# Kernel tuning notes

Hardware: AMD Instinct MI355X
Metric: run time of the kernel (lower is better)

The kernel has to match this reference:

```python
import jax, jax.numpy as jnp
import numpy as np

N, E, F_IN, F_E, EMB, G = 25000, 100000, 32, 8, 32, 512


def _nnconv(x, src, dst, ea, w1, b1, w2, b2, root, bias):
    # edge MLP: [E,F_E] -> [E,16] -> [E, in*EMB] -> per-edge weight matrix [E,in,EMB]
    h = jax.nn.relu(ea @ w1 + b1)
    W = (h @ w2 + b2).reshape(ea.shape[0], x.shape[1], EMB)
    # gather source nodes, per-edge matmul, scatter-add to targets (PyG NNConv, aggr='add')
    msg = jnp.einsum('ei,eio->eo', x[src], W)
    agg = jax.ops.segment_sum(msg, dst, num_segments=x.shape[0])
    return agg + x @ root + bias


def _branch(x, ei, ea, p0, p1):
    x = jax.nn.relu(_nnconv(x, ei[0], ei[1], ea, *p0))
    x = jax.nn.relu(_nnconv(x, ei[0], ei[1], ea, *p1))
    return x


def setup_inputs() -> dict:
    key = jax.random.key(0)
    ks = iter(jax.random.split(key, 64))
    def rnd(shape, s=1.0):
        return jax.random.normal(next(ks), shape, dtype=jnp.float32) * s
    inp = {
        'x_p': rnd((N, F_IN)), 'x_d': rnd((N, F_IN)),
        'edge_attr_p': rnd((E, F_E)), 'edge_attr_d': rnd((E, F_E)),
        'edge_index_p': jax.random.randint(next(ks), (2, E), 0, N),
        'edge_index_d': jax.random.randint(next(ks), (2, E), 0, N),
        'batch_p': jnp.sort(jax.random.randint(next(ks), (N,), 0, G)),
        'batch_d': jnp.sort(jax.random.randint(next(ks), (N,), 0, G)),
    }
    for b in ('p', 'd'):
        inp[b + '_nn0_w1'] = rnd((F_E, 16), 0.1)
        inp[b + '_nn0_b1'] = rnd((16,), 0.1)
        inp[b + '_nn0_w2'] = rnd((16, F_IN * EMB), 0.1)
        inp[b + '_nn0_b2'] = rnd((F_IN * EMB,), 0.1)
        inp[b + '_root0'] = rnd((F_IN, EMB), 0.1)
        inp[b + '_bias0'] = rnd((EMB,), 0.1)
        inp[b + '_nn1_w1'] = rnd((F_E, 16), 0.1)
        inp[b + '_nn1_b1'] = rnd((16,), 0.1)
        inp[b + '_nn1_w2'] = rnd((16, EMB * EMB), 0.1)
        inp[b + '_nn1_b2'] = rnd((EMB * EMB,), 0.1)
        inp[b + '_root1'] = rnd((EMB, EMB), 0.1)
        inp[b + '_bias1'] = rnd((EMB,), 0.1)
    inp['lin0_w'] = rnd((2 * EMB, 2 * EMB), 0.1)
    inp['lin0_b'] = rnd((2 * EMB,), 0.1)
    inp['lin1_w'] = rnd((2 * EMB, 1), 0.1)
    inp['lin1_b'] = rnd((1,), 0.1)
    return inp


def reference(x_p, x_d, edge_attr_p, edge_attr_d, edge_index_p, edge_index_d, batch_p, batch_d,
              p_nn0_w1, p_nn0_b1, p_nn0_w2, p_nn0_b2, p_root0, p_bias0,
              p_nn1_w1, p_nn1_b1, p_nn1_w2, p_nn1_b2, p_root1, p_bias1,
              d_nn0_w1, d_nn0_b1, d_nn0_w2, d_nn0_b2, d_root0, d_bias0,
              d_nn1_w1, d_nn1_b1, d_nn1_w2, d_nn1_b2, d_root1, d_bias1,
              lin0_w, lin0_b, lin1_w, lin1_b):
    p0 = (p_nn0_w1, p_nn0_b1, p_nn0_w2, p_nn0_b2, p_root0, p_bias0)
    p1 = (p_nn1_w1, p_nn1_b1, p_nn1_w2, p_nn1_b2, p_root1, p_bias1)
    d0 = (d_nn0_w1, d_nn0_b1, d_nn0_w2, d_nn0_b2, d_root0, d_bias0)
    d1 = (d_nn1_w1, d_nn1_b1, d_nn1_w2, d_nn1_b2, d_root1, d_bias1)
    hp = _branch(x_p, edge_index_p, edge_attr_p, p0, p1)      # [N, EMB]
    hd = _branch(x_d, edge_index_d, edge_attr_d, d0, d1)      # [N, EMB]
    gp = jax.ops.segment_max(hp, batch_p, num_segments=G)     # global_max_pool
    gd = jax.ops.segment_max(hd, batch_d, num_segments=G)
    x = jnp.concatenate([gp, gd], axis=1)                     # [G, 2*EMB]
    # F.dropout(p=0.5, training=False) is the identity in eval mode
    x = x @ lin0_w + lin0_b
    x = x @ lin1_w + lin1_b                                    # [G, 1]
    return x
```

## Files before the change

kernel.cpp:

```cpp
#include <hip/hip_runtime.h>
#include <hip/hip_bf16.h>

#define NN 25000
#define NE 100000
#define NG 512
#define NPAD 25024
#define NEP 100032
#define NT 6250
#define XL (2 * NPAD * 32)

typedef __attribute__((ext_vector_type(8))) short short8;
typedef __attribute__((ext_vector_type(4))) float f32x4;

__device__ __forceinline__ float bf2f(unsigned short u) {
    union { unsigned u; float f; } v; v.u = (unsigned)u << 16; return v.f;
}
__device__ __forceinline__ unsigned short f2bf(float f) {
    union { __hip_bfloat16 b; unsigned short u; } c;
    c.b = __float2bfloat16(f);
    return c.u;
}
__device__ __forceinline__ unsigned pk2(float lo, float hi) {
    __hip_bfloat162 h2;
    h2.x = __float2bfloat16(lo);
    h2.y = __float2bfloat16(hi);
    union { __hip_bfloat162 h; unsigned u; } c; c.h = h2; return c.u;
}

struct PrepArgs {
    const float* w2[4]; const float* b2[4];
    const float* x0[2];
};
#define S1 (4 * 17 * 1024)
#define S2V (2 * NN * 8)
#define S3 (2 * NN)
#define S4 (NG * 64 / 4)
__global__ __launch_bounds__(256) void prep_kernel(PrepArgs pa,
        unsigned short* __restrict__ Wt, unsigned short* __restrict__ xb,
        int* __restrict__ hist, float* __restrict__ gbuf) {
    int idx = blockIdx.x * 256 + threadIdx.x;
    if (idx < S1) {
        int L = idx / (17 * 1024);
        int r = idx % (17 * 1024);
        int s = r >> 10, o = (r >> 5) & 31, i = r & 31;
        float v = (s < 16) ? pa.w2[L][s * 1024 + i * 32 + o] : pa.b2[L][i * 32 + o];
        Wt[idx] = f2bf(v);
        return;
    }
    idx -= S1;
    if (idx < S2V) {
        int br = idx / (NN * 8);
        int q = idx % (NN * 8);
        float4 v = *(const float4*)(pa.x0[br] + (size_t)q * 4);
        unsigned* dst = (unsigned*)(xb + (size_t)br * NPAD * 32 + (size_t)q * 4);
        dst[0] = pk2(v.x, v.y);
        dst[1] = pk2(v.z, v.w);
        return;
    }
    idx -= S2V;
    if (idx < S3) { hist[idx] = 0; return; }
    idx -= S3;
    if (idx < S4) {
        float4 z = make_float4(0.f, 0.f, 0.f, 0.f);
        *(float4*)(gbuf + (size_t)idx * 4) = z;
    }
}

__global__ __launch_bounds__(256) void hist_kernel(const int* __restrict__ ep,
        const int* __restrict__ ed, int* __restrict__ hist, int* __restrict__ slot) {
    int idx = blockIdx.x * 256 + threadIdx.x;
    if (idx >= 2 * NE) return;
    int br = idx >= NE, e = idx - br * NE;
    const int* ei = br ? ed : ep;
    slot[idx] = atomicAdd(&hist[br * NN + ei[NE + e]], 1);
}

__global__ __launch_bounds__(1024) void scan_kernel(const int* __restrict__ hist,
        int* __restrict__ ptr) {
    int br = blockIdx.x, t = threadIdx.x;
    const int* h = hist + br * NN;
    int* p = ptr + br * (NN + 1);
    int base = t * 25;
    int loc[25]; int s = 0;
    if (base < NN) {
        #pragma unroll
        for (int j = 0; j < 25; ++j) { loc[j] = h[base + j]; s += loc[j]; }
    }
    int w = t >> 6, ln = t & 63;
    int v = s;
    #pragma unroll
    for (int d = 1; d < 64; d <<= 1) {
        int u = __shfl_up(v, d, 64);
        if (ln >= d) v += u;
    }
    __shared__ int wsum[16];
    if (ln == 63) wsum[w] = v;
    __syncthreads();
    if (t < 16) {
        int x = wsum[t];
        #pragma unroll
        for (int d = 1; d < 16; d <<= 1) {
            int u = __shfl_up(x, d, 16);
            if ((t & 15) >= d) x += u;
        }
        wsum[t] = x;
    }
    __syncthreads();
    int run = (w ? wsum[w - 1] : 0) + (v - s);
    if (base < NN) {
        #pragma unroll
        for (int j = 0; j < 25; ++j) { p[base + j] = run; run += loc[j]; }
    }
    if (t == 0) p[NN] = wsum[15];
}

struct EdgeArgs {
    const float* ea[2]; const int* eidx[2];
    const float* w1[2]; const float* b1[2];
};
__global__ __launch_bounds__(256, 2) void edge_kernel(EdgeArgs A, int L,
        const unsigned short* __restrict__ Wt,
        const unsigned short* __restrict__ xb,
        const int* __restrict__ ptr, const int* __restrict__ slot,
        unsigned short* __restrict__ msg) {
    __shared__ unsigned tr[4][256];
    int br = blockIdx.x >> 8;
    int bb = blockIdx.x & 255;
    const float* ea   = A.ea[br];
    const int*   eidx = A.eidx[br];
    const float* w1   = A.w1[br];
    const float* b1   = A.b1[br];
    const unsigned short* W  = Wt + (size_t)(br * 2 + L) * 17 * 1024;
    const unsigned short* xc = xb + (size_t)L * XL + (size_t)br * NPAD * 32;
    const int* pt = ptr + br * (NN + 1);
    const int* sl = slot + br * NE;
    unsigned short* mg = msg + (size_t)br * NEP * 32;

    int tid = threadIdx.x;
    int wv = tid >> 6, lane = tid & 63;
    int lr = lane & 15, kg = lane >> 4;

    short8 WA[17], WB[17];
    #pragma unroll
    for (int s = 0; s < 17; ++s) {
        WA[s] = *(const short8*)(W + (size_t)s * 1024 + lr * 32 + kg * 8);
        WB[s] = *(const short8*)(W + (size_t)s * 1024 + (16 + lr) * 32 + kg * 8);
    }
    float w1r[32], b1r[4];
    #pragma unroll
    for (int r = 0; r < 4; ++r) {
        b1r[r] = b1[kg * 4 + r];
        #pragma unroll
        for (int i = 0; i < 8; ++i) w1r[r * 8 + i] = w1[i * 16 + kg * 4 + r];
    }

    for (int t = bb * 4 + wv; t < NT; t += 1024) {
        int e = t * 16 + lr;
        int src = eidx[e];
        int rk = 0;
        if (kg == 0) rk = pt[eidx[NE + e]] + sl[e];

        short8 xs8 = *(const short8*)(xc + (size_t)src * 32 + kg * 8);
        float xf[8];
        #pragma unroll
        for (int j = 0; j < 8; ++j) xf[j] = bf2f((unsigned short)xs8[j]);

        float4 ea0 = *(const float4*)(ea + (size_t)e * 8);
        float4 ea1 = *(const float4*)(ea + (size_t)e * 8 + 4);
        float hreg[4];
        #pragma unroll
        for (int r = 0; r < 4; ++r) {
            float h = b1r[r];
            h += ea0.x * w1r[r * 8 + 0]; h += ea0.y * w1r[r * 8 + 1];
            h += ea0.z * w1r[r * 8 + 2]; h += ea0.w * w1r[r * 8 + 3];
            h += ea1.x * w1r[r * 8 + 4]; h += ea1.y * w1r[r * 8 + 5];
            h += ea1.z * w1r[r * 8 + 6]; h += ea1.w * w1r[r * 8 + 7];
            hreg[r] = fmaxf(h, 0.f);
        }

        f32x4 acc0 = {0.f, 0.f, 0.f, 0.f}, acc1 = {0.f, 0.f, 0.f, 0.f};
        #pragma unroll
        for (int s = 0; s < 17; ++s) {
            short8 y;
            if (s < 16) {
                float hs = __shfl(hreg[s & 3], lr + ((s >> 2) << 4), 64);
                union { unsigned u[4]; short8 v; } yy;
                yy.u[0] = pk2(hs * xf[0], hs * xf[1]);
                yy.u[1] = pk2(hs * xf[2], hs * xf[3]);
                yy.u[2] = pk2(hs * xf[4], hs * xf[5]);
                yy.u[3] = pk2(hs * xf[6], hs * xf[7]);
                y = yy.v;
            } else {
                y = xs8;
            }
            acc0 = __builtin_amdgcn_mfma_f32_16x16x32_bf16(WA[s], y, acc0, 0, 0, 0);
            acc1 = __builtin_amdgcn_mfma_f32_16x16x32_bf16(WB[s], y, acc1, 0, 0, 0);
        }
        tr[wv][lr * 16 + kg * 2    ] = pk2(acc0[0], acc0[1]);
        tr[wv][lr * 16 + kg * 2 + 1] = pk2(acc0[2], acc0[3]);
        tr[wv][lr * 16 + 8 + kg * 2    ] = pk2(acc1[0], acc1[1]);
        tr[wv][lr * 16 + 8 + kg * 2 + 1] = pk2(acc1[2], acc1[3]);
        int rkb = __shfl(rk, lane >> 2, 64);
        uint4 val = *(uint4*)&tr[wv][(lane >> 2) * 16 + (lane & 3) * 4];
        *(uint4*)(mg + (size_t)rkb * 32 + (lane & 3) * 8) = val;
    }
}

struct GatherArgs { const float* root[2]; const float* bias[2]; const int* batch[2]; };
template<int LAST>
__global__ __launch_bounds__(256) void gather_kernel(GatherArgs G,
        const int* __restrict__ ptr, const unsigned short* __restrict__ msg,
        const unsigned short* __restrict__ xin_, unsigned short* __restrict__ xout_,
        float* __restrict__ gbuf) {
    int gw = (blockIdx.x * 256 + threadIdx.x) >> 5;
    int o = threadIdx.x & 31;
    int br = gw >= NN, n = gw - br * NN;
    const int* p = ptr + br * (NN + 1);
    int lo = p[n], hi = p[n + 1];
    const unsigned short* m = msg + (size_t)br * NEP * 32;
    float sum = 0.f;
    for (int j = lo; j < hi; ++j) sum += bf2f(m[(size_t)j * 32 + o]);
    float xv = bf2f(xin_[(size_t)br * NPAD * 32 + (size_t)n * 32 + o]);
    const float* R = G.root[br];
    float rsum = 0.f;
    #pragma unroll
    for (int i = 0; i < 32; ++i) rsum += __shfl(xv, i, 32) * R[i * 32 + o];
    float v = fmaxf(sum + rsum + G.bias[br][o], 0.f);
    if (!LAST) {
        xout_[(size_t)br * NPAD * 32 + (size_t)n * 32 + o] = f2bf(v);
    } else {
        int g = G.batch[br][n];
        atomicMax((int*)&gbuf[(size_t)g * 64 + br * 32 + o], __float_as_int(v));
    }
}

__global__ __launch_bounds__(64) void final_mlp_kernel(
        const float* __restrict__ gbuf,
        const float* __restrict__ w0, const float* __restrict__ b0,
        const float* __restrict__ w1v, const float* __restrict__ b1v,
        float* __restrict__ out) {
    int g = blockIdx.x;
    int j = threadIdx.x;
    const float* xr = gbuf + (size_t)g * 64;
    float y = b0[j];
    for (int i = 0; i < 64; ++i) y += xr[i] * w0[i * 64 + j];
    float t = y * w1v[j];
    #pragma unroll
    for (int off = 32; off > 0; off >>= 1) t += __shfl_down(t, off, 64);
    if (j == 0) out[g] = t + b1v[0];
}

static size_t aln(size_t v) { return (v + 255) & ~(size_t)255; }

extern "C" void kernel_launch(void* const* d_in, const int* in_sizes, int n_in,
                              void* d_out, int out_size, void* d_ws, size_t ws_size,
                              hipStream_t stream) {
    (void)in_sizes; (void)n_in; (void)out_size; (void)ws_size;
    char* w = (char*)d_ws;
    unsigned short* Wt  = (unsigned short*)w; w += aln((size_t)S1 * 2);
    unsigned short* xb  = (unsigned short*)w; w += aln((size_t)2 * XL * 2);
    unsigned short* msg = (unsigned short*)w; w += aln((size_t)2 * NEP * 32 * 2);
    int* hist = (int*)w; w += aln((size_t)2 * NN * 4);
    int* ptr  = (int*)w; w += aln((size_t)2 * (NN + 1) * 4);
    int* slot = (int*)w; w += aln((size_t)2 * NE * 4);
    float* gbuf = (float*)w; w += aln((size_t)NG * 64 * 4);

    const int* ep = (const int*)d_in[4];
    const int* ed = (const int*)d_in[5];

    PrepArgs pa;
    for (int L4 = 0; L4 < 4; ++L4) {
        int base = 8 + (L4 >> 1) * 12 + (L4 & 1) * 6;
        pa.w2[L4] = (const float*)d_in[base + 2];
        pa.b2[L4] = (const float*)d_in[base + 3];
    }
    pa.x0[0] = (const float*)d_in[0];
    pa.x0[1] = (const float*)d_in[1];
    prep_kernel<<<(S1 + S2V + S3 + S4 + 255) / 256, 256, 0, stream>>>(pa, Wt, xb, hist, gbuf);

    hist_kernel<<<(2 * NE + 255) / 256, 256, 0, stream>>>(ep, ed, hist, slot);
    scan_kernel<<<2, 1024, 0, stream>>>(hist, ptr);

    EdgeArgs ea; GatherArgs ga;
    for (int br = 0; br < 2; ++br) {
        ea.ea[br]    = (const float*)d_in[2 + br];
        ea.eidx[br]  = (const int*)d_in[4 + br];
        ga.batch[br] = (const int*)d_in[6 + br];
    }
    for (int L = 0; L < 2; ++L) {
        for (int br = 0; br < 2; ++br) {
            int base = 8 + br * 12 + L * 6;
            ea.w1[br]   = (const float*)d_in[base + 0];
            ea.b1[br]   = (const float*)d_in[base + 1];
            ga.root[br] = (const float*)d_in[base + 4];
            ga.bias[br] = (const float*)d_in[base + 5];
        }
        edge_kernel<<<512, 256, 0, stream>>>(ea, L, Wt, xb, ptr, slot, msg);
        if (L == 0)
            gather_kernel<0><<<6250, 256, 0, stream>>>(ga, ptr, msg,
                xb, xb + (size_t)XL, gbuf);
        else
            gather_kernel<1><<<6250, 256, 0, stream>>>(ga, ptr, msg,
                xb + (size_t)XL, nullptr, gbuf);
    }

    final_mlp_kernel<<<NG, 64, 0, stream>>>(gbuf,
        (const float*)d_in[32], (const float*)d_in[33],
        (const float*)d_in[34], (const float*)d_in[35],
        (float*)d_out);
}
```

Baseline: 113.0 us.

## Fuse all stages into one cooperative persistent kernel with grid syncs

```diff
diff --git a/kernel.cpp b/kernel.cpp
--- a/kernel.cpp
+++ b/kernel.cpp
@@ -1,5 +1,8 @@
 #include <hip/hip_runtime.h>
 #include <hip/hip_bf16.h>
+#include <hip/hip_cooperative_groups.h>
+
+namespace cg = cooperative_groups;
 
 #define NN 25000
 #define NE 100000
@@ -8,6 +11,7 @@
 #define NEP 100032
 #define NT 6250
 #define XL (2 * NPAD * 32)
+#define BLK 256
 
 typedef __attribute__((ext_vector_type(8))) short short8;
 typedef __attribute__((ext_vector_type(4))) float f32x4;
@@ -27,119 +31,240 @@
     union { __hip_bfloat162 h; unsigned u; } c; c.h = h2; return c.u;
 }
 
-struct PrepArgs {
-    const float* w2[4]; const float* b2[4];
-    const float* x0[2];
-};
 #define S1 (4 * 17 * 1024)
 #define S2V (2 * NN * 8)
 #define S3 (2 * NN)
 #define S4 (NG * 64 / 4)
-__global__ __launch_bounds__(256) void prep_kernel(PrepArgs pa,
-        unsigned short* __restrict__ Wt, unsigned short* __restrict__ xb,
-        int* __restrict__ hist, float* __restrict__ gbuf) {
-    int idx = blockIdx.x * 256 + threadIdx.x;
+
+struct MKArgs {
+    const float* x0[2]; const float* ea[2];
+    const int* eidx[2]; const int* batch[2];
+    const float* w1[4]; const float* b1[4];
+    const float* w2[4]; const float* b2[4];
+    const float* root[4]; const float* bias[4];
+    const float* lw0; const float* lb0; const float* lw1; const float* lb1;
+    float* out;
+    unsigned short* Wt; unsigned short* xb; unsigned short* msg;
+    int* hist; int* ptr; int* slot; float* gbuf;
+};
+
+
+__device__ __forceinline__ void prep_body(const MKArgs& a, int idx) {
     if (idx < S1) {
         int L = idx / (17 * 1024);
         int r = idx % (17 * 1024);
         int s = r >> 10, o = (r >> 5) & 31, i = r & 31;
-        float v = (s < 16) ? pa.w2[L][s * 1024 + i * 32 + o] : pa.b2[L][i * 32 + o];
-        Wt[idx] = f2bf(v);
+        float v = (s < 16) ? a.w2[L][s * 1024 + i * 32 + o] : a.b2[L][i * 32 + o];
+        a.Wt[idx] = f2bf(v);
         return;
     }
     idx -= S1;
     if (idx < S2V) {
         int br = idx / (NN * 8);
         int q = idx % (NN * 8);
-        float4 v = *(const float4*)(pa.x0[br] + (size_t)q * 4);
-        unsigned* dst = (unsigned*)(xb + (size_t)br * NPAD * 32 + (size_t)q * 4);
+        float4 v = *(const float4*)(a.x0[br] + (size_t)q * 4);
+        unsigned* dst = (unsigned*)(a.xb + (size_t)br * NPAD * 32 + (size_t)q * 4);
         dst[0] = pk2(v.x, v.y);
         dst[1] = pk2(v.z, v.w);
         return;
     }
     idx -= S2V;
-    if (idx < S3) { hist[idx] = 0; return; }
+    if (idx < S3) { a.hist[idx] = 0; return; }
     idx -= S3;
-    if (idx < S4) {
-        float4 z = make_float4(0.f, 0.f, 0.f, 0.f);
-        *(float4*)(gbuf + (size_t)idx * 4) = z;
-    }
-}
-
-__global__ __launch_bounds__(256) void hist_kernel(const int* __restrict__ ep,
-        const int* __restrict__ ed, int* __restrict__ hist, int* __restrict__ slot) {
-    int idx = blockIdx.x * 256 + threadIdx.x;
-    if (idx >= 2 * NE) return;
+    if (idx < S4)
+        *(float4*)(a.gbuf + (size_t)idx * 4) = make_float4(0.f, 0.f, 0.f, 0.f);
+}
+
+__device__ __forceinline__ void hist_body(const MKArgs& a, int idx) {
     int br = idx >= NE, e = idx - br * NE;
-    const int* ei = br ? ed : ep;
-    slot[idx] = atomicAdd(&hist[br * NN + ei[NE + e]], 1);
-}
-
-__global__ __launch_bounds__(1024) void scan_kernel(const int* __restrict__ hist,
-        int* __restrict__ ptr) {
-    int br = blockIdx.x, t = threadIdx.x;
-    const int* h = hist + br * NN;
-    int* p = ptr + br * (NN + 1);
-    int base = t * 25;
-    int loc[25]; int s = 0;
-    if (base < NN) {
-        #pragma unroll
-        for (int j = 0; j < 25; ++j) { loc[j] = h[base + j]; s += loc[j]; }
-    }
-    int w = t >> 6, ln = t & 63;
+    a.slot[idx] = atomicAdd(&a.hist[br * NN + a.eidx[br][NE + e]], 1);
+}
+
+__device__ __forceinline__ void scan_body(const MKArgs& a, int br, int tid, int* wsum) {
+    const int* h = a.hist + br * NN;
+    int* p = a.ptr + br * (NN + 1);
+    int base = tid * 98;
+    int s = 0;
+    for (int j = 0; j < 98; ++j) { int ii = base + j; if (ii < NN) s += h[ii]; }
+    int w = tid >> 6, ln = tid & 63;
     int v = s;
     #pragma unroll
-    for (int d = 1; d < 64; d <<= 1) {
-        int u = __shfl_up(v, d, 64);
-        if (ln >= d) v += u;
-    }
-    __shared__ int wsum[16];
+    for (int d = 1; d < 64; d <<= 1) { int u = __shfl_up(v, d, 64); if (ln >= d) v += u; }
     if (ln == 63) wsum[w] = v;
     __syncthreads();
-    if (t < 16) {
-        int x = wsum[t];
-        #pragma unroll
-        for (int d = 1; d < 16; d <<= 1) {
-            int u = __shfl_up(x, d, 16);
-            if ((t & 15) >= d) x += u;
-        }
-        wsum[t] = x;
-    }
-    __syncthreads();
-    int run = (w ? wsum[w - 1] : 0) + (v - s);
-    if (base < NN) {
-        #pragma unroll
-        for (int j = 0; j < 25; ++j) { p[base + j] = run; run += loc[j]; }
-    }
-    if (t == 0) p[NN] = wsum[15];
-}
-
-struct EdgeArgs {
-    const float* ea[2]; const int* eidx[2];
-    const float* w1[2]; const float* b1[2];
-};
-__global__ __launch_bounds__(256, 2) void edge_kernel(EdgeArgs A, int L,
-        const unsigned short* __restrict__ Wt,
-        const unsigned short* __restrict__ xb,
-        const int* __restrict__ ptr, const int* __restrict__ slot,
-        unsigned short* __restrict__ msg) {
+    int run = v - s;
+    for (int k = 0; k < w; ++k) run += wsum[k];
+    for (int j = 0; j < 98; ++j) {
+        int ii = base + j;
+        if (ii < NN) { p[ii] = run; run += h[ii]; }
+    }
+    if (tid == 255) p[NN] = run;
+}
+
+__device__ __forceinline__ void edge_tile(const MKArgs& a, int br, int L, int t,
+        int lr, int kg, int lane, const short8* WA, const short8* WB,
+        const float* w1r, const float* b1r, unsigned* trw) {
+    const int* eidx = a.eidx[br];
+    const unsigned short* xc = a.xb + (size_t)L * XL + (size_t)br * NPAD * 32;
+    int e = t * 16 + lr;
+    int src = eidx[e];
+    int rk = 0;
+    if (kg == 0) rk = a.ptr[br * (NN + 1) + eidx[NE + e]] + a.slot[br * NE + e];
+
+    short8 xs8 = *(const short8*)(xc + (size_t)src * 32 + kg * 8);
+    float xf[8];
+    #pragma unroll
+    for (int j = 0; j < 8; ++j) xf[j] = bf2f((unsigned short)xs8[j]);
+
+    const float* ea = a.ea[br];
+    float4 ea0 = *(const float4*)(ea + (size_t)e * 8);
+    float4 ea1 = *(const float4*)(ea + (size_t)e * 8 + 4);
+    float hreg[4];
+    #pragma unroll
+    for (int r = 0; r < 4; ++r) {
+        float h = b1r[r];
+        h += ea0.x * w1r[r * 8 + 0]; h += ea0.y * w1r[r * 8 + 1];
+        h += ea0.z * w1r[r * 8 + 2]; h += ea0.w * w1r[r * 8 + 3];
+        h += ea1.x * w1r[r * 8 + 4]; h += ea1.y * w1r[r * 8 + 5];
+        h += ea1.z * w1r[r * 8 + 6]; h += ea1.w * w1r[r * 8 + 7];
+        hreg[r] = fmaxf(h, 0.f);
+    }
+
+    f32x4 acc0 = {0.f, 0.f, 0.f, 0.f}, acc1 = {0.f, 0.f, 0.f, 0.f};
+    #pragma unroll
+    for (int s = 0; s < 17; ++s) {
+        short8 y;
+        if (s < 16) {
+            float hs = __shfl(hreg[s & 3], lr + ((s >> 2) << 4), 64);
+            union { unsigned u[4]; short8 v; } yy;
+            yy.u[0] = pk2(hs * xf[0], hs * xf[1]);
+            yy.u[1] = pk2(hs * xf[2], hs * xf[3]);
+            yy.u[2] = pk2(hs * xf[4], hs * xf[5]);
+            yy.u[3] = pk2(hs * xf[6], hs * xf[7]);
+            y = yy.v;
+        } else {
+            y = xs8;
+        }
+        acc0 = __builtin_amdgcn_mfma_f32_16x16x32_bf16(WA[s], y, acc0, 0, 0, 0);
+        acc1 = __builtin_amdgcn_mfma_f32_16x16x32_bf16(WB[s], y, acc1, 0, 0, 0);
+    }
+    trw[lr * 16 + kg * 2    ] = pk2(acc0[0], acc0[1]);
+    trw[lr * 16 + kg * 2 + 1] = pk2(acc0[2], acc0[3]);
+    trw[lr * 16 + 8 + kg * 2    ] = pk2(acc1[0], acc1[1]);
+    trw[lr * 16 + 8 + kg * 2 + 1] = pk2(acc1[2], acc1[3]);
+    int rkb = __shfl(rk, lane >> 2, 64);
+    uint4 val = *(uint4*)&trw[(lane >> 2) * 16 + (lane & 3) * 4];
+    unsigned short* mg = a.msg + (size_t)br * NEP * 32;
+    *(uint4*)(mg + (size_t)rkb * 32 + (lane & 3) * 8) = val;
+}
+
+__device__ __forceinline__ void gather_body(const MKArgs& a, int L, int gw, int o) {
+    int br = gw >= NN, n = gw - br * NN;
+    int k4 = br * 2 + L;
+    const int* p = a.ptr + br * (NN + 1);
+    int lo = p[n], hi = p[n + 1];
+    const unsigned short* m = a.msg + (size_t)br * NEP * 32;
+    float sum = 0.f;
+    for (int j = lo; j < hi; ++j) sum += bf2f(m[(size_t)j * 32 + o]);
+    float xv = bf2f(a.xb[(size_t)L * XL + ((size_t)br * NPAD + n) * 32 + o]);
+    const float* R = a.root[k4];
+    float rsum = 0.f;
+    #pragma unroll
+    for (int i = 0; i < 32; ++i) rsum += __shfl(xv, i, 32) * R[i * 32 + o];
+    float v = fmaxf(sum + rsum + a.bias[k4][o], 0.f);
+    if (L == 0) {
+        a.xb[(size_t)XL + ((size_t)br * NPAD + n) * 32 + o] = f2bf(v);
+    } else {
+        atomicMax((int*)&a.gbuf[(size_t)a.batch[br][n] * 64 + br * 32 + o],
+                  __float_as_int(v));
+    }
+}
+
+__device__ __forceinline__ void final_body(const MKArgs& a, int g, int j) {
+    const float* xr = a.gbuf + (size_t)g * 64;
+    float y = a.lb0[j];
+    for (int i = 0; i < 64; ++i) y += xr[i] * a.lw0[i * 64 + j];
+    float t = y * a.lw1[j];
+    #pragma unroll
+    for (int off = 32; off > 0; off >>= 1) t += __shfl_down(t, off, 64);
+    if (j == 0) a.out[g] = t + a.lb1[0];
+}
+
+__global__ __launch_bounds__(BLK, 2) void mega_kernel(MKArgs a) {
+    cg::grid_group grid = cg::this_grid();
     __shared__ unsigned tr[4][256];
-    int br = blockIdx.x >> 8;
-    int bb = blockIdx.x & 255;
-    const float* ea   = A.ea[br];
-    const int*   eidx = A.eidx[br];
-    const float* w1   = A.w1[br];
-    const float* b1   = A.b1[br];
-    const unsigned short* W  = Wt + (size_t)(br * 2 + L) * 17 * 1024;
-    const unsigned short* xc = xb + (size_t)L * XL + (size_t)br * NPAD * 32;
-    const int* pt = ptr + br * (NN + 1);
-    const int* sl = slot + br * NE;
-    unsigned short* mg = msg + (size_t)br * NEP * 32;
-
+    __shared__ int wsum[4];
+    const int tid = threadIdx.x;
+    const int bid = blockIdx.x;
+    const int nb  = gridDim.x;
+    const int gs  = nb * BLK;
+    const int gtid = bid * BLK + tid;
+
+    for (int idx = gtid; idx < S1 + S2V + S3 + S4; idx += gs) prep_body(a, idx);
+    grid.sync();
+
+    for (int idx = gtid; idx < 2 * NE; idx += gs) hist_body(a, idx);
+    grid.sync();
+
+    if (bid < 2) scan_body(a, bid, tid, wsum);
+    grid.sync();
+
+    int wv = tid >> 6, lane = tid & 63;
+    int lr = lane & 15, kg = lane >> 4;
+    int br = bid & 1, bb2 = bid >> 1;
+    int strideT = (nb >> 1) * 4;
+
+    for (int L = 0; L < 2; ++L) {
+        {
+            int k4 = br * 2 + L;
+            const unsigned short* W = a.Wt + (size_t)k4 * 17 * 1024;
+            short8 WA[17], WB[17];
+            #pragma unroll
+            for (int s = 0; s < 17; ++s) {
+                WA[s] = *(const short8*)(W + (size_t)s * 1024 + lr * 32 + kg * 8);
+                WB[s] = *(const short8*)(W + (size_t)s * 1024 + (16 + lr) * 32 + kg * 8);
+            }
+            float w1r[32], b1r[4];
+            #pragma unroll
+            for (int r = 0; r < 4; ++r) {
+                b1r[r] = a.b1[k4][kg * 4 + r];
+                #pragma unroll
+                for (int i = 0; i < 8; ++i) w1r[r * 8 + i] = a.w1[k4][i * 16 + kg * 4 + r];
+            }
+            for (int t = bb2 * 4 + wv; t < NT; t += strideT)
+                edge_tile(a, br, L, t, lr, kg, lane, WA, WB, w1r, b1r, tr[wv]);
+        }
+        grid.sync();
+
+        for (int gw = gtid >> 5; gw < 2 * NN; gw += gs / 32)
+            gather_body(a, L, gw, tid & 31);
+        grid.sync();
+    }
+
+    if (tid < 64)
+        for (int g = bid; g < NG; g += nb) final_body(a, g, tid);
+}
+
+__global__ __launch_bounds__(256) void fb_prep(MKArgs a) {
+    int idx = blockIdx.x * 256 + threadIdx.x;
+    if (idx < S1 + S2V + S3 + S4) prep_body(a, idx);
+}
+__global__ __launch_bounds__(256) void fb_hist(MKArgs a) {
+    int idx = blockIdx.x * 256 + threadIdx.x;
+    if (idx < 2 * NE) hist_body(a, idx);
+}
+__global__ __launch_bounds__(256) void fb_scan(MKArgs a) {
+    __shared__ int wsum[4];
+    scan_body(a, blockIdx.x, threadIdx.x, wsum);
+}
+__global__ __launch_bounds__(256, 2) void fb_edge(MKArgs a, int L) {
+    __shared__ unsigned tr[4][256];
     int tid = threadIdx.x;
     int wv = tid >> 6, lane = tid & 63;
     int lr = lane & 15, kg = lane >> 4;
-
+    int br = blockIdx.x >> 8, bb = blockIdx.x & 255;
+    int k4 = br * 2 + L;
+    const unsigned short* W = a.Wt + (size_t)k4 * 17 * 1024;
     short8 WA[17], WB[17];
     #pragma unroll
     for (int s = 0; s < 17; ++s) {
@@ -149,105 +274,19 @@
     float w1r[32], b1r[4];
     #pragma unroll
     for (int r = 0; r < 4; ++r) {
-        b1r[r] = b1[kg * 4 + r];
+        b1r[r] = a.b1[k4][kg * 4 + r];
         #pragma unroll
-        for (int i = 0; i < 8; ++i) w1r[r * 8 + i] = w1[i * 16 + kg * 4 + r];
-    }
-
-    for (int t = bb * 4 + wv; t < NT; t += 1024) {
-        int e = t * 16 + lr;
-        int src = eidx[e];
-        int rk = 0;
-        if (kg == 0) rk = pt[eidx[NE + e]] + sl[e];
-
-        short8 xs8 = *(const short8*)(xc + (size_t)src * 32 + kg * 8);
-        float xf[8];
-        #pragma unroll
-        for (int j = 0; j < 8; ++j) xf[j] = bf2f((unsigned short)xs8[j]);
-
-        float4 ea0 = *(const float4*)(ea + (size_t)e * 8);
-        float4 ea1 = *(const float4*)(ea + (size_t)e * 8 + 4);
-        float hreg[4];
-        #pragma unroll
-        for (int r = 0; r < 4; ++r) {
-            float h = b1r[r];
-            h += ea0.x * w1r[r * 8 + 0]; h += ea0.y * w1r[r * 8 + 1];
-            h += ea0.z * w1r[r * 8 + 2]; h += ea0.w * w1r[r * 8 + 3];
-            h += ea1.x * w1r[r * 8 + 4]; h += ea1.y * w1r[r * 8 + 5];
-            h += ea1.z * w1r[r * 8 + 6]; h += ea1.w * w1r[r * 8 + 7];
-            hreg[r] = fmaxf(h, 0.f);
-        }
-
-        f32x4 acc0 = {0.f, 0.f, 0.f, 0.f}, acc1 = {0.f, 0.f, 0.f, 0.f};
-        #pragma unroll
-        for (int s = 0; s < 17; ++s) {
-            short8 y;
-            if (s < 16) {
-                float hs = __shfl(hreg[s & 3], lr + ((s >> 2) << 4), 64);
-                union { unsigned u[4]; short8 v; } yy;
-                yy.u[0] = pk2(hs * xf[0], hs * xf[1]);
-                yy.u[1] = pk2(hs * xf[2], hs * xf[3]);
-                yy.u[2] = pk2(hs * xf[4], hs * xf[5]);
-                yy.u[3] = pk2(hs * xf[6], hs * xf[7]);
-                y = yy.v;
-            } else {
-                y = xs8;
-            }
-            acc0 = __builtin_amdgcn_mfma_f32_16x16x32_bf16(WA[s], y, acc0, 0, 0, 0);
-            acc1 = __builtin_amdgcn_mfma_f32_16x16x32_bf16(WB[s], y, acc1, 0, 0, 0);
-        }
-        tr[wv][lr * 16 + kg * 2    ] = pk2(acc0[0], acc0[1]);
-        tr[wv][lr * 16 + kg * 2 + 1] = pk2(acc0[2], acc0[3]);
-        tr[wv][lr * 16 + 8 + kg * 2    ] = pk2(acc1[0], acc1[1]);
-        tr[wv][lr * 16 + 8 + kg * 2 + 1] = pk2(acc1[2], acc1[3]);
-        int rkb = __shfl(rk, lane >> 2, 64);
-        uint4 val = *(uint4*)&tr[wv][(lane >> 2) * 16 + (lane & 3) * 4];
-        *(uint4*)(mg + (size_t)rkb * 32 + (lane & 3) * 8) = val;
-    }
-}
-
-struct GatherArgs { const float* root[2]; const float* bias[2]; const int* batch[2]; };
-template<int LAST>
-__global__ __launch_bounds__(256) void gather_kernel(GatherArgs G,
-        const int* __restrict__ ptr, const unsigned short* __restrict__ msg,
-        const unsigned short* __restrict__ xin_, unsigned short* __restrict__ xout_,
-        float* __restrict__ gbuf) {
+        for (int i = 0; i < 8; ++i) w1r[r * 8 + i] = a.w1[k4][i * 16 + kg * 4 + r];
+    }
+    for (int t = bb * 4 + wv; t < NT; t += 1024)
+        edge_tile(a, br, L, t, lr, kg, lane, WA, WB, w1r, b1r, tr[wv]);
+}
+__global__ __launch_bounds__(256) void fb_gather(MKArgs a, int L) {
     int gw = (blockIdx.x * 256 + threadIdx.x) >> 5;
-    int o = threadIdx.x & 31;
-    int br = gw >= NN, n = gw - br * NN;
-    const int* p = ptr + br * (NN + 1);
-    int lo = p[n], hi = p[n + 1];
-    const unsigned short* m = msg + (size_t)br * NEP * 32;
-    float sum = 0.f;
-    for (int j = lo; j < hi; ++j) sum += bf2f(m[(size_t)j * 32 + o]);
-    float xv = bf2f(xin_[(size_t)br * NPAD * 32 + (size_t)n * 32 + o]);
-    const float* R = G.root[br];
-    float rsum = 0.f;
-    #pragma unroll
-    for (int i = 0; i < 32; ++i) rsum += __shfl(xv, i, 32) * R[i * 32 + o];
-    float v = fmaxf(sum + rsum + G.bias[br][o], 0.f);
-    if (!LAST) {
-        xout_[(size_t)br * NPAD * 32 + (size_t)n * 32 + o] = f2bf(v);
-    } else {
-        int g = G.batch[br][n];
-        atomicMax((int*)&gbuf[(size_t)g * 64 + br * 32 + o], __float_as_int(v));
-    }
-}
-
-__global__ __launch_bounds__(64) void final_mlp_kernel(
-        const float* __restrict__ gbuf,
-        const float* __restrict__ w0, const float* __restrict__ b0,
-        const float* __restrict__ w1v, const float* __restrict__ b1v,
-        float* __restrict__ out) {
-    int g = blockIdx.x;
-    int j = threadIdx.x;
-    const float* xr = gbuf + (size_t)g * 64;
-    float y = b0[j];
-    for (int i = 0; i < 64; ++i) y += xr[i] * w0[i * 64 + j];
-    float t = y * w1v[j];
-    #pragma unroll
-    for (int off = 32; off > 0; off >>= 1) t += __shfl_down(t, off, 64);
-    if (j == 0) out[g] = t + b1v[0];
+    if (gw < 2 * NN) gather_body(a, L, gw, threadIdx.x & 31);
+}
+__global__ __launch_bounds__(64) void fb_final(MKArgs a) {
+    final_body(a, blockIdx.x, threadIdx.x);
 }
 
 static size_t aln(size_t v) { return (v + 255) & ~(size_t)255; }
@@ -265,47 +304,59 @@
     int* slot = (int*)w; w += aln((size_t)2 * NE * 4);
     float* gbuf = (float*)w; w += aln((size_t)NG * 64 * 4);
 
-    const int* ep = (const int*)d_in[4];
-    const int* ed = (const int*)d_in[5];
-
-    PrepArgs pa;
-    for (int L4 = 0; L4 < 4; ++L4) {
-        int base = 8 + (L4 >> 1) * 12 + (L4 & 1) * 6;
-        pa.w2[L4] = (const float*)d_in[base + 2];
-        pa.b2[L4] = (const float*)d_in[base + 3];
-    }
-    pa.x0[0] = (const float*)d_in[0];
-    pa.x0[1] = (const float*)d_in[1];
-    prep_kernel<<<(S1 + S2V + S3 + S4 + 255) / 256, 256, 0, stream>>>(pa, Wt, xb, hist, gbuf);
-
-    hist_kernel<<<(2 * NE + 255) / 256, 256, 0, stream>>>(ep, ed, hist, slot);
-    scan_kernel<<<2, 1024, 0, stream>>>(hist, ptr);
-
-    EdgeArgs ea; GatherArgs ga;
+    MKArgs a;
     for (int br = 0; br < 2; ++br) {
-        ea.ea[br]    = (const float*)d_in[2 + br];
-        ea.eidx[br]  = (const int*)d_in[4 + br];
-        ga.batch[br] = (const int*)d_in[6 + br];
-    }
-    for (int L = 0; L < 2; ++L) {
-        for (int br = 0; br < 2; ++br) {
+        a.x0[br]    = (const float*)d_in[br];
+        a.ea[br]    = (const float*)d_in[2 + br];
+        a.eidx[br]  = (const int*)d_in[4 + br];
+        a.batch[br] = (const int*)d_in[6 + br];
+        for (int L = 0; L < 2; ++L) {
             int base = 8 + br * 12 + L * 6;
-            ea.w1[br]   = (const float*)d_in[base + 0];
-            ea.b1[br]   = (const float*)d_in[base + 1];
-            ga.root[br] = (const float*)d_in[base + 4];
-            ga.bias[br] = (const float*)d_in[base + 5];
-        }
-        edge_kernel<<<512, 256, 0, stream>>>(ea, L, Wt, xb, ptr, slot, msg);
-        if (L == 0)
-            gather_kernel<0><<<6250, 256, 0, stream>>>(ga, ptr, msg,
-                xb, xb + (size_t)XL, gbuf);
-        else
-            gather_kernel<1><<<6250, 256, 0, stream>>>(ga, ptr, msg,
-                xb + (size_t)XL, nullptr, gbuf);
-    }
-
-    final_mlp_kernel<<<NG, 64, 0, stream>>>(gbuf,
-        (const float*)d_in[32], (const float*)d_in[33],
-        (const float*)d_in[34], (const float*)d_in[35],
-        (float*)d_out);
-}
+            int k = br * 2 + L;
+            a.w1[k]   = (const float*)d_in[base + 0];
+            a.b1[k]   = (const float*)d_in[base + 1];
+            a.w2[k]   = (const float*)d_in[base + 2];
+            a.b2[k]   = (const float*)d_in[base + 3];
+            a.root[k] = (const float*)d_in[base + 4];
+            a.bias[k] = (const float*)d_in[base + 5];
+        }
+    }
+    a.lw0 = (const float*)d_in[32];
+    a.lb0 = (const float*)d_in[33];
+    a.lw1 = (const float*)d_in[34];
+    a.lb1 = (const float*)d_in[35];
+    a.out = (float*)d_out;
+    a.Wt = Wt; a.xb = xb; a.msg = msg;
+    a.hist = hist; a.ptr = ptr; a.slot = slot; a.gbuf = gbuf;
+
+    bool coop_done = false;
+    int maxBlk = 0;
+    hipError_t qerr = hipOccupancyMaxActiveBlocksPerMultiprocessor(&maxBlk, mega_kernel, BLK, 0);
+    if (qerr == hipSuccess && maxBlk >= 1) {
+        hipDeviceProp_t props;
+        int dev = 0;
+        if (hipGetDevice(&dev) == hipSuccess &&
+            hipGetDeviceProperties(&props, dev) == hipSuccess) {
+            long g = (long)maxBlk * props.multiProcessorCount;
+            if (g > 512) g = 512;
+            g &= ~1L;
+            if (g >= 2) {
+                void* params[] = { (void*)&a };
+                hipError_t e = hipLaunchCooperativeKernel(mega_kernel,
+                        dim3((unsigned)g), dim3(BLK), params, 0u, stream);
+                coop_done = (e == hipSuccess);
+            }
+        }
+    }
+
+    if (!coop_done) {
+        fb_prep<<<(S1 + S2V + S3 + S4 + 255) / 256, 256, 0, stream>>>(a);
+        fb_hist<<<(2 * NE + 255) / 256, 256, 0, stream>>>(a);
+        fb_scan<<<2, 256, 0, stream>>>(a);
+        for (int L = 0; L < 2; ++L) {
+            fb_edge<<<512, 256, 0, stream>>>(a, L);
+            fb_gather<<<6250, 256, 0, stream>>>(a, L);
+        }
+        fb_final<<<NG, 64, 0, stream>>>(a);
+    }
+}
```

After: 446.8 us. 295% more time.
